# Optimization experiments

Measured on AMD Instinct MI355X. Metric: run time of the kernel, lower is better.

## Reference

```python
import jax, jax.numpy as jnp
import numpy as np

N = 100000
E = 1600000
D_IN = 128
D_HID = 128


def setup_inputs() -> dict:
    key = jax.random.key(0)
    ks = jax.random.split(key, 10)
    x = jax.random.normal(ks[0], (N, D_IN), dtype=jnp.float32)
    edge_index = jax.random.randint(ks[1], (2, E), 0, N, dtype=jnp.int64)
    def lin(k, i, o):
        kw, kb = jax.random.split(k)
        s = 1.0 / np.sqrt(i)
        return (jax.random.uniform(kw, (o, i), jnp.float32, -s, s),
                jax.random.uniform(kb, (o,), jnp.float32, -s, s))
    w0a, b0a = lin(ks[2], D_IN, D_HID)
    w0b, b0b = lin(ks[3], D_HID, D_HID)
    w1a, b1a = lin(ks[4], D_HID, D_HID)
    w1b, b1b = lin(ks[5], D_HID, D_HID)
    return {"x": x, "edge_index": edge_index,
            "w0a": w0a, "b0a": b0a, "w0b": w0b, "b0b": b0b,
            "w1a": w1a, "b1a": b1a, "w1b": w1b, "b1b": b1b}


def _gin_layer(x, src, dst, wa, ba, wb, bb):
    # GINConv, eps=0: h_i = x_i + sum_{j in N(i)} x_j (messages from src aggregated at dst)
    agg = jax.ops.segment_sum(x[src], dst, num_segments=N)  # [N, D]
    h = x + agg
    h = jax.nn.relu(h @ wa.T + ba)  # LinearBlock (no bn, no dropout)
    return h @ wb.T + bb            # final Linear of local_nn


def reference(x, edge_index, w0a, b0a, w0b, b0b, w1a, b1a, w1b, b1b):
    src, dst = edge_index[0], edge_index[1]
    h = _gin_layer(x, src, dst, w0a, b0a, w0b, b0b)
    h = _gin_layer(h, src, dst, w1a, b1a, w1b, b1b)
    return h
```

## Files before the change

### kernel.cpp

```cpp
#include <hip/hip_runtime.h>


typedef __attribute__((ext_vector_type(8))) short bf16x8;
typedef __attribute__((ext_vector_type(4))) float floatx4;
typedef __attribute__((ext_vector_type(2))) float floatx2;

#define WS_ALIGN(x) (((x) + 255) & ~(size_t)255)
#define NBMAX 400
#define BCAP 6144

__device__ __forceinline__ unsigned short f2b(float f) {
  unsigned u = __builtin_bit_cast(unsigned, f);
  u = (u + 0x7FFF + ((u >> 16) & 1)) >> 16;
  return (unsigned short)u;
}

__device__ __forceinline__ floatx2 bpair(unsigned d) {
  floatx2 r;
  r[0] = __builtin_bit_cast(float, d << 16);
  r[1] = __builtin_bit_cast(float, d & 0xffff0000u);
  return r;
}

__global__ __launch_bounds__(256) void bucket_split(const int* __restrict__ src,
                                                    const int* __restrict__ dst,
                                                    int* __restrict__ bcnt,
                                                    unsigned* __restrict__ barr, int E, int nb) {
  __shared__ int cnt[NBMAX], base[NBMAX], cur[NBMAX];
  int t = threadIdx.x;
  for (int i = t; i < nb; i += 256) { cnt[i] = 0; cur[i] = 0; }
  __syncthreads();
  int e0 = blockIdx.x * 8192;
  int s[32], d[32];
#pragma unroll
  for (int k = 0; k < 32; k++) {
    int e = e0 + k * 256 + t;
    if (e < E) { s[k] = src[e]; d[k] = dst[e]; } else { d[k] = -1; }
  }
#pragma unroll
  for (int k = 0; k < 32; k++)
    if (d[k] >= 0) atomicAdd(&cnt[d[k] >> 8], 1);
  __syncthreads();
  for (int i = t; i < nb; i += 256) base[i] = cnt[i] ? atomicAdd(&bcnt[i], cnt[i]) : 0;
  __syncthreads();
#pragma unroll
  for (int k = 0; k < 32; k++)
    if (d[k] >= 0) {
      int b = d[k] >> 8;
      int r = atomicAdd(&cur[b], 1);
      barr[(size_t)b * BCAP + base[b] + r] = ((unsigned)(d[k] & 255) << 17) | (unsigned)s[k];
    }
}

__global__ void bucket_scan(const int* __restrict__ bcnt, int* __restrict__ sbase, int nb,
                            int* __restrict__ rowptr, int n) {
  __shared__ int buf[512];
  int t = threadIdx.x;
  int v = (t < nb) ? bcnt[t] : 0;
  buf[t] = v;
  __syncthreads();
  for (int off = 1; off < 512; off <<= 1) {
    int add = (t >= off) ? buf[t - off] : 0;
    __syncthreads();
    buf[t] += add;
    __syncthreads();
  }
  if (t < nb) sbase[t] = buf[t] - v;
  if (t == nb - 1) { sbase[nb] = buf[t]; rowptr[n] = buf[t]; }
}

__global__ __launch_bounds__(256) void bucket_csr(const unsigned* __restrict__ barr,
                                                  const int* __restrict__ bcnt,
                                                  const int* __restrict__ sbase,
                                                  int* __restrict__ rowptr, int* __restrict__ srt,
                                                  int n) {
  __shared__ int cnt[256], off[256], off2[256];
  int b = blockIdx.x, t = threadIdx.x;
  int cb = bcnt[b];
  int node0 = b * 256;
  int nlocal = min(256, n - node0);
  cnt[t] = 0;
  off2[t] = 0;
  __syncthreads();
  const unsigned* bp = barr + (size_t)b * BCAP;
  for (int i = t; i < cb; i += 256) atomicAdd(&cnt[bp[i] >> 17], 1);
  __syncthreads();
  int v = cnt[t];
  off[t] = v;
  __syncthreads();
  for (int o = 1; o < 256; o <<= 1) {
    int add = (t >= o) ? off[t - o] : 0;
    __syncthreads();
    off[t] += add;
    __syncthreads();
  }
  int excl = off[t] - v;
  int sb = sbase[b];
  if (t < nlocal) rowptr[node0 + t] = sb + excl;
  cnt[t] = excl;
  __syncthreads();
  for (int i = t; i < cb; i += 256) {
    unsigned pk = bp[i];
    int local = pk >> 17;
    int r = atomicAdd(&off2[local], 1);
    srt[sb + cnt[local] + r] = pk & 0x1FFFF;
  }
}

__global__ void cvt_kernel(const float* __restrict__ x, unsigned short* __restrict__ xb, int n4) {
  int i = blockIdx.x * blockDim.x + threadIdx.x;
  if (i < n4) {
    float4 v = ((const float4*)x)[i];
    uint2 pk;
    pk.x = (unsigned)f2b(v.x) | ((unsigned)f2b(v.y) << 16);
    pk.y = (unsigned)f2b(v.z) | ((unsigned)f2b(v.w) << 16);
    ((uint2*)xb)[i] = pk;
  }
}

__global__ __launch_bounds__(256) void aggregate_bf16(const unsigned short* __restrict__ X,
                                                      const int* __restrict__ rowptr,
                                                      const int* __restrict__ srt,
                                                      unsigned short* __restrict__ out, int n) {
  int w = blockIdx.x * 4 + (threadIdx.x >> 6);
  if (w >= n) return;
  int lane = threadIdx.x & 63;
  int c = lane & 15;
  int s = lane >> 4;
  const uint4* Xv = (const uint4*)X;

  int p0 = rowptr[w], e = rowptr[w + 1];
  int deg = e - p0;
  int trips = (deg + 3) >> 2;

  uint4 uself = {0, 0, 0, 0};
  if (s == 0) uself = Xv[(size_t)w * 16 + c];

  floatx2 acc2[4];
#pragma unroll
  for (int i = 0; i < 4; i++) acc2[i] = floatx2{0.f, 0.f};

  for (int g = 0; g < trips; g += 4) {
    int idx[4];
    bool val[4];
#pragma unroll
    for (int k = 0; k < 4; k++) {
      int j = (g + k) * 4 + s;
      val[k] = j < deg;
      idx[k] = srt[p0 + (val[k] ? j : 0)];
    }
    uint4 u[4];
#pragma unroll
    for (int k = 0; k < 4; k++) u[k] = Xv[(size_t)idx[k] * 16 + c];
#pragma unroll
    for (int k = 0; k < 4; k++) {
      if (!val[k]) { u[k].x = 0; u[k].y = 0; u[k].z = 0; u[k].w = 0; }
      acc2[0] += bpair(u[k].x);
      acc2[1] += bpair(u[k].y);
      acc2[2] += bpair(u[k].z);
      acc2[3] += bpair(u[k].w);
    }
  }

  acc2[0] += bpair(uself.x);
  acc2[1] += bpair(uself.y);
  acc2[2] += bpair(uself.z);
  acc2[3] += bpair(uself.w);

#pragma unroll
  for (int i = 0; i < 4; i++) {
#pragma unroll
    for (int h = 0; h < 2; h++) {
      acc2[i][h] += __shfl_xor(acc2[i][h], 16, 64);
      acc2[i][h] += __shfl_xor(acc2[i][h], 32, 64);
    }
  }

  unsigned pk = (unsigned)f2b(acc2[s][0]) | ((unsigned)f2b(acc2[s][1]) << 16);
  ((unsigned*)out)[(size_t)w * 64 + c * 4 + s] = pk;
}

__device__ __forceinline__ void stage_w(char* buf, const float* __restrict__ W, int t) {
  for (int idx = t; idx < 2048; idx += 512) {
    int nrow = idx >> 4, c = idx & 15;
    float4 a = ((const float4*)W)[idx * 2];
    float4 b = ((const float4*)W)[idx * 2 + 1];
    uint4 pk;
    pk.x = (unsigned)f2b(a.x) | ((unsigned)f2b(a.y) << 16);
    pk.y = (unsigned)f2b(a.z) | ((unsigned)f2b(a.w) << 16);
    pk.z = (unsigned)f2b(b.x) | ((unsigned)f2b(b.y) << 16);
    pk.w = (unsigned)f2b(b.z) | ((unsigned)f2b(b.w) << 16);
    *(uint4*)(buf + nrow * 256 + ((c ^ (nrow & 15)) << 4)) = pk;
  }
}

template <int OUT_BF16>
__global__ __launch_bounds__(512) void mlp_kernel(
    const unsigned short* __restrict__ A, const float* __restrict__ Wa,
    const float* __restrict__ ba, const float* __restrict__ Wb,
    const float* __restrict__ bb, void* __restrict__ Cout, int n) {
  __shared__ __align__(16) char lds[65536];
  char* bufA = lds;
  char* bufB = lds + 32768;
  int t = threadIdx.x;
  stage_w(bufA, Wa, t);
  stage_w(bufB, Wb, t);

  int wave = t >> 6, lane = t & 63;
  int m = lane & 15, q = lane >> 4;
  int rbase = blockIdx.x * 128;
  int rowA = rbase + wave * 16 + m;
  int rA = rowA < n ? rowA : (n - 1);

  bf16x8 af[4];
  const bf16x8* Arow = (const bf16x8*)(A + (size_t)rA * 128);
#pragma unroll
  for (int ks = 0; ks < 4; ks++) af[ks] = Arow[ks * 4 + q];

  __syncthreads();

  floatx4 acc[8];
  floatx4 zf = {0.f, 0.f, 0.f, 0.f};
#pragma unroll
  for (int j = 0; j < 8; j++) acc[j] = zf;
#pragma unroll
  for (int ks = 0; ks < 4; ks++) {
#pragma unroll
    for (int j = 0; j < 8; j++) {
      bf16x8 bf = *(const bf16x8*)(bufA + (j * 16 + m) * 256 + (((ks * 4 + q) ^ m) << 4));
      acc[j] = __builtin_amdgcn_mfma_f32_16x16x32_bf16(af[ks], bf, acc[j], 0, 0, 0);
    }
  }
  __syncthreads();

#pragma unroll
  for (int j = 0; j < 8; j++) {
    float bias = ba[j * 16 + m];
#pragma unroll
    for (int reg = 0; reg < 4; reg++) {
      float v = fmaxf(acc[j][reg] + bias, 0.f);
      int lr = wave * 16 + q * 4 + reg;
      int col = j * 16 + m;
      *(unsigned short*)(bufA + lr * 256 + (((col >> 3) ^ (lr & 15)) << 4) + (col & 7) * 2) =
          f2b(v);
    }
  }
  __syncthreads();

  int lrA = wave * 16 + m;
#pragma unroll
  for (int ks = 0; ks < 4; ks++)
    af[ks] = *(const bf16x8*)(bufA + lrA * 256 + (((ks * 4 + q) ^ m) << 4));
#pragma unroll
  for (int j = 0; j < 8; j++) acc[j] = zf;
#pragma unroll
  for (int ks = 0; ks < 4; ks++) {
#pragma unroll
    for (int j = 0; j < 8; j++) {
      bf16x8 bf = *(const bf16x8*)(bufB + (j * 16 + m) * 256 + (((ks * 4 + q) ^ m) << 4));
      acc[j] = __builtin_amdgcn_mfma_f32_16x16x32_bf16(af[ks], bf, acc[j], 0, 0, 0);
    }
  }

#pragma unroll
  for (int j = 0; j < 8; j++) {
    float bias = bb[j * 16 + m];
#pragma unroll
    for (int reg = 0; reg < 4; reg++) {
      int row = rbase + wave * 16 + q * 4 + reg;
      if (row >= n) continue;
      float v = acc[j][reg] + bias;
      int col = j * 16 + m;
      if (OUT_BF16)
        ((unsigned short*)Cout)[(size_t)row * 128 + col] = f2b(v);
      else
        ((float*)Cout)[(size_t)row * 128 + col] = v;
    }
  }
}

extern "C" void kernel_launch(void* const* d_in, const int* in_sizes, int n_in,
                              void* d_out, int out_size, void* d_ws, size_t ws_size,
                              hipStream_t stream) {
  const float* x   = (const float*)d_in[0];
  const int*   ei  = (const int*)d_in[1];
  const float* w0a = (const float*)d_in[2];
  const float* b0a = (const float*)d_in[3];
  const float* w0b = (const float*)d_in[4];
  const float* b0b = (const float*)d_in[5];
  const float* w1a = (const float*)d_in[6];
  const float* b1a = (const float*)d_in[7];
  const float* w1b = (const float*)d_in[8];
  const float* b1b = (const float*)d_in[9];
  float* out = (float*)d_out;

  int n = in_sizes[0] / 128;
  int E = in_sizes[1] / 2;
  const int* src = ei;
  const int* dst = ei + E;
  int nb = (n + 255) / 256;

  char* w = (char*)d_ws;
  int* rowptr = (int*)w;           w += WS_ALIGN((size_t)(n + 1) * 4);
  int* sbase = (int*)w;            w += WS_ALIGN((size_t)(NBMAX + 1) * 4);
  int* bcnt = (int*)w;             w += WS_ALIGN((size_t)NBMAX * 4);
  int* srt = (int*)w;              w += WS_ALIGN((size_t)E * 4);
  unsigned short* xb = (unsigned short*)w;  w += WS_ALIGN((size_t)n * 128 * 2);
  unsigned* barr = (unsigned*)w;
  unsigned short* B1 = (unsigned short*)w;

  hipMemsetAsync(bcnt, 0, (size_t)nb * 4, stream);
  bucket_split<<<(E + 8191) / 8192, 256, 0, stream>>>(src, dst, bcnt, barr, E, nb);
  bucket_scan<<<1, 512, 0, stream>>>(bcnt, sbase, nb, rowptr, n);
  bucket_csr<<<nb, 256, 0, stream>>>(barr, bcnt, sbase, rowptr, srt, n);

  cvt_kernel<<<(n * 32 + 255) / 256, 256, 0, stream>>>(x, xb, n * 32);

  int agg_grid = (n + 3) / 4;
  int mlp_grid = (n + 127) / 128;

  aggregate_bf16<<<agg_grid, 256, 0, stream>>>(xb, rowptr, srt, B1, n);
  mlp_kernel<1><<<mlp_grid, 512, 0, stream>>>(B1, w0a, b0a, w0b, b0b, xb, n);

  aggregate_bf16<<<agg_grid, 256, 0, stream>>>(xb, rowptr, srt, B1, n);
  mlp_kernel<0><<<mlp_grid, 512, 0, stream>>>(B1, w1a, b1a, w1b, b1b, out, n);
}
```

Before: 331.4 us.

## Store bf16 features in column-chunk-major layout and split aggregation by feature chunk

Features are now stored transposed into 16-byte column chunks (chunk-major, node-minor), written that way by a new conversion kernel, by the aggregation and by the first MLP's output. Aggregation blocks now each handle one pair of chunks for 32 nodes, so each chunk slice of the feature table (about 3.2 MB) is small enough to stay cache-resident while gathering, instead of random 256-byte rows spread over the whole table. In exchange, edge indices are re-read 8 times (once per chunk group), lanes in a wave loop to the maximum degree among their 8 nodes, and the transposed conversion and MLP loads/stores become strided and less coalesced.

```diff
diff --git a/kernel.cpp b/kernel.cpp
--- a/kernel.cpp
+++ b/kernel.cpp
@@ -4,6 +4,7 @@
 typedef __attribute__((ext_vector_type(8))) short bf16x8;
 typedef __attribute__((ext_vector_type(4))) float floatx4;
 typedef __attribute__((ext_vector_type(2))) float floatx2;
+typedef __attribute__((ext_vector_type(4))) unsigned uintx4;
 
 #define WS_ALIGN(x) (((x) + 255) & ~(size_t)255)
 #define NBMAX 400
@@ -107,59 +108,70 @@
   }
 }
 
-__global__ void cvt_kernel(const float* __restrict__ x, unsigned short* __restrict__ xb, int n4) {
-  int i = blockIdx.x * blockDim.x + threadIdx.x;
-  if (i < n4) {
-    float4 v = ((const float4*)x)[i];
-    uint2 pk;
-    pk.x = (unsigned)f2b(v.x) | ((unsigned)f2b(v.y) << 16);
-    pk.y = (unsigned)f2b(v.z) | ((unsigned)f2b(v.w) << 16);
-    ((uint2*)xb)[i] = pk;
-  }
-}
-
-__global__ __launch_bounds__(256) void aggregate_bf16(const unsigned short* __restrict__ X,
+__global__ __launch_bounds__(256) void cvt_t_kernel(const float* __restrict__ x,
+                                                    uintx4* __restrict__ xbT, int n) {
+  int r = blockIdx.x * 256 + threadIdx.x;
+  bool ok = r < n;
+  int rr = ok ? r : 0;
+  const float4* xv = (const float4*)x;
+#pragma unroll 4
+  for (int c = 0; c < 16; c++) {
+    float4 a = xv[(size_t)rr * 32 + c * 2];
+    float4 b = xv[(size_t)rr * 32 + c * 2 + 1];
+    uintx4 pk;
+    pk.x = (unsigned)f2b(a.x) | ((unsigned)f2b(a.y) << 16);
+    pk.y = (unsigned)f2b(a.z) | ((unsigned)f2b(a.w) << 16);
+    pk.z = (unsigned)f2b(b.x) | ((unsigned)f2b(b.y) << 16);
+    pk.w = (unsigned)f2b(b.z) | ((unsigned)f2b(b.w) << 16);
+    if (ok) xbT[(size_t)c * n + r] = pk;
+  }
+}
+
+__global__ __launch_bounds__(256) void aggregate_bf16(const uintx4* __restrict__ XT,
                                                       const int* __restrict__ rowptr,
                                                       const int* __restrict__ srt,
-                                                      unsigned short* __restrict__ out, int n) {
-  int w = blockIdx.x * 4 + (threadIdx.x >> 6);
-  if (w >= n) return;
+                                                      uintx4* __restrict__ OT, int n) {
+  int p = blockIdx.x & 7;
+  int g = blockIdx.x >> 3;
   int lane = threadIdx.x & 63;
-  int c = lane & 15;
+  int wave = threadIdx.x >> 6;
   int s = lane >> 4;
-  const uint4* Xv = (const uint4*)X;
-
-  int p0 = rowptr[w], e = rowptr[w + 1];
-  int deg = e - p0;
-  int trips = (deg + 3) >> 2;
-
-  uint4 uself = {0, 0, 0, 0};
-  if (s == 0) uself = Xv[(size_t)w * 16 + c];
+  int nl = (lane >> 1) & 7;
+  int h = lane & 1;
+  int node = g * 32 + wave * 8 + nl;
+  bool live = node < n;
+  int nd = live ? node : 0;
+  const uintx4* Xc = XT + (size_t)(p * 2 + h) * n;
+
+  int p0 = rowptr[nd];
+  int deg = live ? (rowptr[nd + 1] - p0) : 0;
+
+  int dmax = deg;
+  dmax = max(dmax, __shfl_xor(dmax, 2, 64));
+  dmax = max(dmax, __shfl_xor(dmax, 4, 64));
+  dmax = max(dmax, __shfl_xor(dmax, 8, 64));
+  int trips = (dmax + 3) >> 2;
+
+  uintx4 uself = {0, 0, 0, 0};
+  if (s == 0 && live) uself = Xc[nd];
 
   floatx2 acc2[4];
 #pragma unroll
   for (int i = 0; i < 4; i++) acc2[i] = floatx2{0.f, 0.f};
 
-  for (int g = 0; g < trips; g += 4) {
-    int idx[4];
-    bool val[4];
-#pragma unroll
-    for (int k = 0; k < 4; k++) {
-      int j = (g + k) * 4 + s;
-      val[k] = j < deg;
-      idx[k] = srt[p0 + (val[k] ? j : 0)];
-    }
-    uint4 u[4];
-#pragma unroll
-    for (int k = 0; k < 4; k++) u[k] = Xv[(size_t)idx[k] * 16 + c];
-#pragma unroll
-    for (int k = 0; k < 4; k++) {
-      if (!val[k]) { u[k].x = 0; u[k].y = 0; u[k].z = 0; u[k].w = 0; }
-      acc2[0] += bpair(u[k].x);
-      acc2[1] += bpair(u[k].y);
-      acc2[2] += bpair(u[k].z);
-      acc2[3] += bpair(u[k].w);
-    }
+  for (int i = 0; i < trips; i += 2) {
+    int j0 = s + 4 * i, j1 = j0 + 4;
+    bool v0 = j0 < deg, v1 = j1 < deg;
+    int i0 = __builtin_nontemporal_load(srt + p0 + (v0 ? j0 : 0));
+    int i1 = __builtin_nontemporal_load(srt + p0 + (v1 ? j1 : 0));
+    uintx4 u0 = Xc[i0];
+    uintx4 u1 = Xc[i1];
+    if (!v0) u0 = uintx4{0, 0, 0, 0};
+    if (!v1) u1 = uintx4{0, 0, 0, 0};
+    acc2[0] += bpair(u0.x); acc2[1] += bpair(u0.y);
+    acc2[2] += bpair(u0.z); acc2[3] += bpair(u0.w);
+    acc2[0] += bpair(u1.x); acc2[1] += bpair(u1.y);
+    acc2[2] += bpair(u1.z); acc2[3] += bpair(u1.w);
   }
 
   acc2[0] += bpair(uself.x);
@@ -170,14 +182,20 @@
 #pragma unroll
   for (int i = 0; i < 4; i++) {
 #pragma unroll
-    for (int h = 0; h < 2; h++) {
-      acc2[i][h] += __shfl_xor(acc2[i][h], 16, 64);
-      acc2[i][h] += __shfl_xor(acc2[i][h], 32, 64);
-    }
-  }
-
-  unsigned pk = (unsigned)f2b(acc2[s][0]) | ((unsigned)f2b(acc2[s][1]) << 16);
-  ((unsigned*)out)[(size_t)w * 64 + c * 4 + s] = pk;
+    for (int k = 0; k < 2; k++) {
+      acc2[i][k] += __shfl_xor(acc2[i][k], 16, 64);
+      acc2[i][k] += __shfl_xor(acc2[i][k], 32, 64);
+    }
+  }
+
+  if (s == 0 && live) {
+    uintx4 pk;
+    pk.x = (unsigned)f2b(acc2[0][0]) | ((unsigned)f2b(acc2[0][1]) << 16);
+    pk.y = (unsigned)f2b(acc2[1][0]) | ((unsigned)f2b(acc2[1][1]) << 16);
+    pk.z = (unsigned)f2b(acc2[2][0]) | ((unsigned)f2b(acc2[2][1]) << 16);
+    pk.w = (unsigned)f2b(acc2[3][0]) | ((unsigned)f2b(acc2[3][1]) << 16);
+    __builtin_nontemporal_store(pk, OT + (size_t)(p * 2 + h) * n + node);
+  }
 }
 
 __device__ __forceinline__ void stage_w(char* buf, const float* __restrict__ W, int t) {
@@ -213,9 +231,9 @@
   int rA = rowA < n ? rowA : (n - 1);
 
   bf16x8 af[4];
-  const bf16x8* Arow = (const bf16x8*)(A + (size_t)rA * 128);
-#pragma unroll
-  for (int ks = 0; ks < 4; ks++) af[ks] = Arow[ks * 4 + q];
+  const bf16x8* AT = (const bf16x8*)A;
+#pragma unroll
+  for (int ks = 0; ks < 4; ks++) af[ks] = AT[(size_t)(ks * 4 + q) * n + rA];
 
   __syncthreads();
 
@@ -272,7 +290,7 @@
       float v = acc[j][reg] + bias;
       int col = j * 16 + m;
       if (OUT_BF16)
-        ((unsigned short*)Cout)[(size_t)row * 128 + col] = f2b(v);
+        ((unsigned short*)Cout)[((size_t)(col >> 3) * n + row) * 8 + (col & 7)] = f2b(v);
       else
         ((float*)Cout)[(size_t)row * 128 + col] = v;
     }
@@ -314,14 +332,14 @@
   bucket_scan<<<1, 512, 0, stream>>>(bcnt, sbase, nb, rowptr, n);
   bucket_csr<<<nb, 256, 0, stream>>>(barr, bcnt, sbase, rowptr, srt, n);
 
-  cvt_kernel<<<(n * 32 + 255) / 256, 256, 0, stream>>>(x, xb, n * 32);
-
-  int agg_grid = (n + 3) / 4;
+  cvt_t_kernel<<<(n + 255) / 256, 256, 0, stream>>>(x, (uintx4*)xb, n);
+
+  int agg_grid = ((n + 31) / 32) * 8;
   int mlp_grid = (n + 127) / 128;
 
-  aggregate_bf16<<<agg_grid, 256, 0, stream>>>(xb, rowptr, srt, B1, n);
+  aggregate_bf16<<<agg_grid, 256, 0, stream>>>((const uintx4*)xb, rowptr, srt, (uintx4*)B1, n);
   mlp_kernel<1><<<mlp_grid, 512, 0, stream>>>(B1, w0a, b0a, w0b, b0b, xb, n);
 
-  aggregate_bf16<<<agg_grid, 256, 0, stream>>>(xb, rowptr, srt, B1, n);
+  aggregate_bf16<<<agg_grid, 256, 0, stream>>>((const uintx4*)xb, rowptr, srt, (uintx4*)B1, n);
   mlp_kernel<0><<<mlp_grid, 512, 0, stream>>>(B1, w1a, b1a, w1b, b1b, out, n);
 }
```

New measurement: 599.0 us. 80.7% more time.

## Pad CSR rows to multiples of four with self-loop and zero-row sentinels

Applied to the files above, without the earlier changes.

Builds the CSR with each node's row padded to a multiple of four, inserting the node itself as a self-loop entry and pointing padding entries at an extra zeroed feature row. The aggregation kernel then runs a simple unmasked gather loop driven by a per-node padded degree, with no validity checks and no separate self-feature load. This trades some extra gathers and index storage, plus padding writes in CSR construction, for simpler control flow in the hot loop.

```diff
diff --git a/kernel.cpp b/kernel.cpp
--- a/kernel.cpp
+++ b/kernel.cpp
@@ -4,6 +4,7 @@
 typedef __attribute__((ext_vector_type(8))) short bf16x8;
 typedef __attribute__((ext_vector_type(4))) float floatx4;
 typedef __attribute__((ext_vector_type(2))) float floatx2;
+typedef __attribute__((ext_vector_type(4))) unsigned uintx4;
 
 #define WS_ALIGN(x) (((x) + 255) & ~(size_t)255)
 #define NBMAX 400
@@ -56,7 +57,7 @@
                             int* __restrict__ rowptr, int n) {
   __shared__ int buf[512];
   int t = threadIdx.x;
-  int v = (t < nb) ? bcnt[t] : 0;
+  int v = (t < nb) ? (bcnt[t] + 1024) : 0;
   buf[t] = v;
   __syncthreads();
   for (int off = 1; off < 512; off <<= 1) {
@@ -72,8 +73,9 @@
 __global__ __launch_bounds__(256) void bucket_csr(const unsigned* __restrict__ barr,
                                                   const int* __restrict__ bcnt,
                                                   const int* __restrict__ sbase,
-                                                  int* __restrict__ rowptr, int* __restrict__ srt,
-                                                  int n) {
+                                                  int* __restrict__ rowptr,
+                                                  int* __restrict__ degp,
+                                                  int* __restrict__ srt, int n) {
   __shared__ int cnt[256], off[256], off2[256];
   int b = blockIdx.x, t = threadIdx.x;
   int cb = bcnt[b];
@@ -86,7 +88,8 @@
   for (int i = t; i < cb; i += 256) atomicAdd(&cnt[bp[i] >> 17], 1);
   __syncthreads();
   int v = cnt[t];
-  off[t] = v;
+  int vp = (v + 4) & ~3;
+  off[t] = vp;
   __syncthreads();
   for (int o = 1; o < 256; o <<= 1) {
     int add = (t >= o) ? off[t - o] : 0;
@@ -94,9 +97,12 @@
     off[t] += add;
     __syncthreads();
   }
-  int excl = off[t] - v;
+  int excl = off[t] - vp;
   int sb = sbase[b];
-  if (t < nlocal) rowptr[node0 + t] = sb + excl;
+  if (t < nlocal) {
+    rowptr[node0 + t] = sb + excl;
+    degp[node0 + t] = vp;
+  }
   cnt[t] = excl;
   __syncthreads();
   for (int i = t; i < cb; i += 256) {
@@ -104,6 +110,11 @@
     int local = pk >> 17;
     int r = atomicAdd(&off2[local], 1);
     srt[sb + cnt[local] + r] = pk & 0x1FFFF;
+  }
+  if (t < nlocal) {
+    int base = sb + excl;
+    srt[base + v] = node0 + t;
+    for (int i = v + 1; i < vp; i++) srt[base + i] = n;
   }
 }
 
@@ -118,66 +129,45 @@
   }
 }
 
-__global__ __launch_bounds__(256) void aggregate_bf16(const unsigned short* __restrict__ X,
+__global__ __launch_bounds__(256) void aggregate_bf16(const uintx4* __restrict__ Xv,
                                                       const int* __restrict__ rowptr,
+                                                      const int* __restrict__ degp,
                                                       const int* __restrict__ srt,
-                                                      unsigned short* __restrict__ out, int n) {
+                                                      unsigned* __restrict__ out, int n) {
   int w = blockIdx.x * 4 + (threadIdx.x >> 6);
   if (w >= n) return;
   int lane = threadIdx.x & 63;
   int c = lane & 15;
   int s = lane >> 4;
-  const uint4* Xv = (const uint4*)X;
-
-  int p0 = rowptr[w], e = rowptr[w + 1];
-  int deg = e - p0;
-  int trips = (deg + 3) >> 2;
-
-  uint4 uself = {0, 0, 0, 0};
-  if (s == 0) uself = Xv[(size_t)w * 16 + c];
+
+  int p0 = rowptr[w] + s;
+  int trips = degp[w] >> 2;
 
   floatx2 acc2[4];
 #pragma unroll
   for (int i = 0; i < 4; i++) acc2[i] = floatx2{0.f, 0.f};
 
-  for (int g = 0; g < trips; g += 4) {
-    int idx[4];
-    bool val[4];
-#pragma unroll
-    for (int k = 0; k < 4; k++) {
-      int j = (g + k) * 4 + s;
-      val[k] = j < deg;
-      idx[k] = srt[p0 + (val[k] ? j : 0)];
-    }
-    uint4 u[4];
-#pragma unroll
-    for (int k = 0; k < 4; k++) u[k] = Xv[(size_t)idx[k] * 16 + c];
-#pragma unroll
-    for (int k = 0; k < 4; k++) {
-      if (!val[k]) { u[k].x = 0; u[k].y = 0; u[k].z = 0; u[k].w = 0; }
-      acc2[0] += bpair(u[k].x);
-      acc2[1] += bpair(u[k].y);
-      acc2[2] += bpair(u[k].z);
-      acc2[3] += bpair(u[k].w);
-    }
-  }
-
-  acc2[0] += bpair(uself.x);
-  acc2[1] += bpair(uself.y);
-  acc2[2] += bpair(uself.z);
-  acc2[3] += bpair(uself.w);
+#pragma unroll 4
+  for (int i = 0; i < trips; i++) {
+    int r = srt[p0 + 4 * i];
+    uintx4 u = Xv[(size_t)r * 16 + c];
+    acc2[0] += bpair(u.x);
+    acc2[1] += bpair(u.y);
+    acc2[2] += bpair(u.z);
+    acc2[3] += bpair(u.w);
+  }
 
 #pragma unroll
   for (int i = 0; i < 4; i++) {
 #pragma unroll
-    for (int h = 0; h < 2; h++) {
-      acc2[i][h] += __shfl_xor(acc2[i][h], 16, 64);
-      acc2[i][h] += __shfl_xor(acc2[i][h], 32, 64);
+    for (int k = 0; k < 2; k++) {
+      acc2[i][k] += __shfl_xor(acc2[i][k], 16, 64);
+      acc2[i][k] += __shfl_xor(acc2[i][k], 32, 64);
     }
   }
 
   unsigned pk = (unsigned)f2b(acc2[s][0]) | ((unsigned)f2b(acc2[s][1]) << 16);
-  ((unsigned*)out)[(size_t)w * 64 + c * 4 + s] = pk;
+  out[(size_t)w * 64 + c * 4 + s] = pk;
 }
 
 __device__ __forceinline__ void stage_w(char* buf, const float* __restrict__ W, int t) {
@@ -304,24 +294,28 @@
   int* rowptr = (int*)w;           w += WS_ALIGN((size_t)(n + 1) * 4);
   int* sbase = (int*)w;            w += WS_ALIGN((size_t)(NBMAX + 1) * 4);
   int* bcnt = (int*)w;             w += WS_ALIGN((size_t)NBMAX * 4);
-  int* srt = (int*)w;              w += WS_ALIGN((size_t)E * 4);
-  unsigned short* xb = (unsigned short*)w;  w += WS_ALIGN((size_t)n * 128 * 2);
+  int* degp = (int*)w;             w += WS_ALIGN((size_t)n * 4);
+  int* srt = (int*)w;              w += WS_ALIGN(((size_t)E + NBMAX * 1024 + 1024) * 4);
+  unsigned short* xb = (unsigned short*)w;  w += WS_ALIGN((size_t)(n + 1) * 128 * 2);
   unsigned* barr = (unsigned*)w;
   unsigned short* B1 = (unsigned short*)w;
 
   hipMemsetAsync(bcnt, 0, (size_t)nb * 4, stream);
+  hipMemsetAsync(xb + (size_t)n * 128, 0, 256, stream);
   bucket_split<<<(E + 8191) / 8192, 256, 0, stream>>>(src, dst, bcnt, barr, E, nb);
   bucket_scan<<<1, 512, 0, stream>>>(bcnt, sbase, nb, rowptr, n);
-  bucket_csr<<<nb, 256, 0, stream>>>(barr, bcnt, sbase, rowptr, srt, n);
+  bucket_csr<<<nb, 256, 0, stream>>>(barr, bcnt, sbase, rowptr, degp, srt, n);
 
   cvt_kernel<<<(n * 32 + 255) / 256, 256, 0, stream>>>(x, xb, n * 32);
 
   int agg_grid = (n + 3) / 4;
   int mlp_grid = (n + 127) / 128;
 
-  aggregate_bf16<<<agg_grid, 256, 0, stream>>>(xb, rowptr, srt, B1, n);
+  aggregate_bf16<<<agg_grid, 256, 0, stream>>>((const uintx4*)xb, rowptr, degp, srt,
+                                               (unsigned*)B1, n);
   mlp_kernel<1><<<mlp_grid, 512, 0, stream>>>(B1, w0a, b0a, w0b, b0b, xb, n);
 
-  aggregate_bf16<<<agg_grid, 256, 0, stream>>>(xb, rowptr, srt, B1, n);
+  aggregate_bf16<<<agg_grid, 256, 0, stream>>>((const uintx4*)xb, rowptr, degp, srt,
+                                               (unsigned*)B1, n);
   mlp_kernel<0><<<mlp_grid, 512, 0, stream>>>(B1, w1a, b1a, w1b, b1b, out, n);
 }
```

New measurement: 340.6 us. 1.03x slower.

## Fuse prep work, drop scan kernel and memset, pre-convert weights once

Applied to the files above, without the earlier changes.

Merges the x-to-bf16 conversion, the bucket-count zeroing and a one-time bf16 conversion of all four weight matrices into a single prep kernel. This removes the memset and the separate cvt launch. The standalone bucket scan kernel is removed; each CSR block instead reduces the preceding bucket counts itself to find its base offset. MLP blocks now copy pre-converted bf16 weights into LDS rather than converting fp32 per block, at the cost of redundant per-block prefix reductions.

```diff
diff --git a/kernel.cpp b/kernel.cpp
--- a/kernel.cpp
+++ b/kernel.cpp
@@ -4,6 +4,7 @@
 typedef __attribute__((ext_vector_type(8))) short bf16x8;
 typedef __attribute__((ext_vector_type(4))) float floatx4;
 typedef __attribute__((ext_vector_type(2))) float floatx2;
+typedef __attribute__((ext_vector_type(4))) unsigned uintx4;
 
 #define WS_ALIGN(x) (((x) + 255) & ~(size_t)255)
 #define NBMAX 400
@@ -20,6 +21,37 @@
   r[0] = __builtin_bit_cast(float, d << 16);
   r[1] = __builtin_bit_cast(float, d & 0xffff0000u);
   return r;
+}
+
+__global__ __launch_bounds__(256) void prep_kernel(const float* __restrict__ x,
+                                                   unsigned short* __restrict__ xb,
+                                                   const float* __restrict__ w0a,
+                                                   const float* __restrict__ w0b,
+                                                   const float* __restrict__ w1a,
+                                                   const float* __restrict__ w1b,
+                                                   uintx4* __restrict__ wb16,
+                                                   int* __restrict__ bcnt, int n4) {
+  int i = blockIdx.x * 256 + threadIdx.x;
+  if (i < n4) {
+    float4 v = ((const float4*)x)[i];
+    uint2 pk;
+    pk.x = (unsigned)f2b(v.x) | ((unsigned)f2b(v.y) << 16);
+    pk.y = (unsigned)f2b(v.z) | ((unsigned)f2b(v.w) << 16);
+    ((uint2*)xb)[i] = pk;
+  }
+  if (i < 8192) {
+    const float* W = (i < 2048) ? w0a : (i < 4096) ? w0b : (i < 6144) ? w1a : w1b;
+    int j = i & 2047;
+    float4 a = ((const float4*)W)[j * 2];
+    float4 b = ((const float4*)W)[j * 2 + 1];
+    uintx4 pk;
+    pk.x = (unsigned)f2b(a.x) | ((unsigned)f2b(a.y) << 16);
+    pk.y = (unsigned)f2b(a.z) | ((unsigned)f2b(a.w) << 16);
+    pk.z = (unsigned)f2b(b.x) | ((unsigned)f2b(b.y) << 16);
+    pk.w = (unsigned)f2b(b.z) | ((unsigned)f2b(b.w) << 16);
+    wb16[i] = pk;
+  }
+  if (i < NBMAX) bcnt[i] = 0;
 }
 
 __global__ __launch_bounds__(256) void bucket_split(const int* __restrict__ src,
@@ -52,36 +84,27 @@
     }
 }
 
-__global__ void bucket_scan(const int* __restrict__ bcnt, int* __restrict__ sbase, int nb,
-                            int* __restrict__ rowptr, int n) {
-  __shared__ int buf[512];
-  int t = threadIdx.x;
-  int v = (t < nb) ? bcnt[t] : 0;
-  buf[t] = v;
-  __syncthreads();
-  for (int off = 1; off < 512; off <<= 1) {
-    int add = (t >= off) ? buf[t - off] : 0;
-    __syncthreads();
-    buf[t] += add;
-    __syncthreads();
-  }
-  if (t < nb) sbase[t] = buf[t] - v;
-  if (t == nb - 1) { sbase[nb] = buf[t]; rowptr[n] = buf[t]; }
-}
-
 __global__ __launch_bounds__(256) void bucket_csr(const unsigned* __restrict__ barr,
                                                   const int* __restrict__ bcnt,
-                                                  const int* __restrict__ sbase,
                                                   int* __restrict__ rowptr, int* __restrict__ srt,
-                                                  int n) {
-  __shared__ int cnt[256], off[256], off2[256];
+                                                  int n, int nb) {
+  __shared__ int cnt[256], off[256], off2[256], red[256];
   int b = blockIdx.x, t = threadIdx.x;
   int cb = bcnt[b];
   int node0 = b * 256;
   int nlocal = min(256, n - node0);
   cnt[t] = 0;
   off2[t] = 0;
-  __syncthreads();
+  int partial = 0;
+  for (int i = t; i < b; i += 256) partial += bcnt[i];
+  red[t] = partial;
+  __syncthreads();
+  for (int o = 128; o > 0; o >>= 1) {
+    if (t < o) red[t] += red[t + o];
+    __syncthreads();
+  }
+  int sb = red[0];
+
   const unsigned* bp = barr + (size_t)b * BCAP;
   for (int i = t; i < cb; i += 256) atomicAdd(&cnt[bp[i] >> 17], 1);
   __syncthreads();
@@ -95,7 +118,6 @@
     __syncthreads();
   }
   int excl = off[t] - v;
-  int sb = sbase[b];
   if (t < nlocal) rowptr[node0 + t] = sb + excl;
   cnt[t] = excl;
   __syncthreads();
@@ -105,17 +127,7 @@
     int r = atomicAdd(&off2[local], 1);
     srt[sb + cnt[local] + r] = pk & 0x1FFFF;
   }
-}
-
-__global__ void cvt_kernel(const float* __restrict__ x, unsigned short* __restrict__ xb, int n4) {
-  int i = blockIdx.x * blockDim.x + threadIdx.x;
-  if (i < n4) {
-    float4 v = ((const float4*)x)[i];
-    uint2 pk;
-    pk.x = (unsigned)f2b(v.x) | ((unsigned)f2b(v.y) << 16);
-    pk.y = (unsigned)f2b(v.z) | ((unsigned)f2b(v.w) << 16);
-    ((uint2*)xb)[i] = pk;
-  }
+  if (b == nb - 1 && t == 0) rowptr[n] = sb + cb;
 }
 
 __global__ __launch_bounds__(256) void aggregate_bf16(const unsigned short* __restrict__ X,
@@ -127,13 +139,13 @@
   int lane = threadIdx.x & 63;
   int c = lane & 15;
   int s = lane >> 4;
-  const uint4* Xv = (const uint4*)X;
+  const uintx4* Xv = (const uintx4*)X;
 
   int p0 = rowptr[w], e = rowptr[w + 1];
   int deg = e - p0;
   int trips = (deg + 3) >> 2;
 
-  uint4 uself = {0, 0, 0, 0};
+  uintx4 uself = {0, 0, 0, 0};
   if (s == 0) uself = Xv[(size_t)w * 16 + c];
 
   floatx2 acc2[4];
@@ -149,12 +161,12 @@
       val[k] = j < deg;
       idx[k] = srt[p0 + (val[k] ? j : 0)];
     }
-    uint4 u[4];
+    uintx4 u[4];
 #pragma unroll
     for (int k = 0; k < 4; k++) u[k] = Xv[(size_t)idx[k] * 16 + c];
 #pragma unroll
     for (int k = 0; k < 4; k++) {
-      if (!val[k]) { u[k].x = 0; u[k].y = 0; u[k].z = 0; u[k].w = 0; }
+      if (!val[k]) u[k] = uintx4{0, 0, 0, 0};
       acc2[0] += bpair(u[k].x);
       acc2[1] += bpair(u[k].y);
       acc2[2] += bpair(u[k].z);
@@ -170,9 +182,9 @@
 #pragma unroll
   for (int i = 0; i < 4; i++) {
 #pragma unroll
-    for (int h = 0; h < 2; h++) {
-      acc2[i][h] += __shfl_xor(acc2[i][h], 16, 64);
-      acc2[i][h] += __shfl_xor(acc2[i][h], 32, 64);
+    for (int k = 0; k < 2; k++) {
+      acc2[i][k] += __shfl_xor(acc2[i][k], 16, 64);
+      acc2[i][k] += __shfl_xor(acc2[i][k], 32, 64);
     }
   }
 
@@ -180,31 +192,25 @@
   ((unsigned*)out)[(size_t)w * 64 + c * 4 + s] = pk;
 }
 
-__device__ __forceinline__ void stage_w(char* buf, const float* __restrict__ W, int t) {
+__device__ __forceinline__ void stage_wb(char* buf, const uintx4* __restrict__ Wb, int t) {
   for (int idx = t; idx < 2048; idx += 512) {
     int nrow = idx >> 4, c = idx & 15;
-    float4 a = ((const float4*)W)[idx * 2];
-    float4 b = ((const float4*)W)[idx * 2 + 1];
-    uint4 pk;
-    pk.x = (unsigned)f2b(a.x) | ((unsigned)f2b(a.y) << 16);
-    pk.y = (unsigned)f2b(a.z) | ((unsigned)f2b(a.w) << 16);
-    pk.z = (unsigned)f2b(b.x) | ((unsigned)f2b(b.y) << 16);
-    pk.w = (unsigned)f2b(b.z) | ((unsigned)f2b(b.w) << 16);
-    *(uint4*)(buf + nrow * 256 + ((c ^ (nrow & 15)) << 4)) = pk;
+    uintx4 pk = Wb[idx];
+    *(uintx4*)(buf + nrow * 256 + ((c ^ (nrow & 15)) << 4)) = pk;
   }
 }
 
 template <int OUT_BF16>
 __global__ __launch_bounds__(512) void mlp_kernel(
-    const unsigned short* __restrict__ A, const float* __restrict__ Wa,
-    const float* __restrict__ ba, const float* __restrict__ Wb,
+    const unsigned short* __restrict__ A, const uintx4* __restrict__ Wa16,
+    const float* __restrict__ ba, const uintx4* __restrict__ Wb16,
     const float* __restrict__ bb, void* __restrict__ Cout, int n) {
   __shared__ __align__(16) char lds[65536];
   char* bufA = lds;
   char* bufB = lds + 32768;
   int t = threadIdx.x;
-  stage_w(bufA, Wa, t);
-  stage_w(bufB, Wb, t);
+  stage_wb(bufA, Wa16, t);
+  stage_wb(bufB, Wb16, t);
 
   int wave = t >> 6, lane = t & 63;
   int m = lane & 15, q = lane >> 4;
@@ -302,26 +308,26 @@
 
   char* w = (char*)d_ws;
   int* rowptr = (int*)w;           w += WS_ALIGN((size_t)(n + 1) * 4);
-  int* sbase = (int*)w;            w += WS_ALIGN((size_t)(NBMAX + 1) * 4);
   int* bcnt = (int*)w;             w += WS_ALIGN((size_t)NBMAX * 4);
   int* srt = (int*)w;              w += WS_ALIGN((size_t)E * 4);
   unsigned short* xb = (unsigned short*)w;  w += WS_ALIGN((size_t)n * 128 * 2);
+  uintx4* wb16 = (uintx4*)w;       w += WS_ALIGN((size_t)8192 * 16);
   unsigned* barr = (unsigned*)w;
   unsigned short* B1 = (unsigned short*)w;
 
-  hipMemsetAsync(bcnt, 0, (size_t)nb * 4, stream);
+  int n4 = n * 32;
+
+  prep_kernel<<<(n4 + 255) / 256, 256, 0, stream>>>(x, xb, w0a, w0b, w1a, w1b, wb16, bcnt, n4);
+
   bucket_split<<<(E + 8191) / 8192, 256, 0, stream>>>(src, dst, bcnt, barr, E, nb);
-  bucket_scan<<<1, 512, 0, stream>>>(bcnt, sbase, nb, rowptr, n);
-  bucket_csr<<<nb, 256, 0, stream>>>(barr, bcnt, sbase, rowptr, srt, n);
-
-  cvt_kernel<<<(n * 32 + 255) / 256, 256, 0, stream>>>(x, xb, n * 32);
+  bucket_csr<<<nb, 256, 0, stream>>>(barr, bcnt, rowptr, srt, n, nb);
 
   int agg_grid = (n + 3) / 4;
   int mlp_grid = (n + 127) / 128;
 
-  aggregate_bf16<<<agg_grid, 256, 0, stream>>>(xb, rowptr, srt, B1, n);
-  mlp_kernel<1><<<mlp_grid, 512, 0, stream>>>(B1, w0a, b0a, w0b, b0b, xb, n);
-
-  aggregate_bf16<<<agg_grid, 256, 0, stream>>>(xb, rowptr, srt, B1, n);
-  mlp_kernel<0><<<mlp_grid, 512, 0, stream>>>(B1, w1a, b1a, w1b, b1b, out, n);
-}
+  aggregate_bf16<<<agg_grid, 256, 0, stream>>>(xb, rowptr, srt, (unsigned short*)B1, n);
+  mlp_kernel<1><<<mlp_grid, 512, 0, stream>>>(B1, wb16, b0a, wb16 + 2048, b0b, xb, n);
+
+  aggregate_bf16<<<agg_grid, 256, 0, stream>>>(xb, rowptr, srt, (unsigned short*)B1, n);
+  mlp_kernel<0><<<mlp_grid, 512, 0, stream>>>(B1, wb16 + 4096, b1a, wb16 + 6144, b1b, out, n);
+}
```

Measured after the change: 320.0 us. 1.04x faster.
